# Kernel optimization log

Hardware: AMD Instinct MI355X
Metric: run time of the kernel (lower is better)

The kernel has to match this reference:

```python
import jax, jax.numpy as jnp
import numpy as np


def setup_inputs() -> dict:
    key = jax.random.key(0)
    k0, k1, k2, k3, k4, k5 = jax.random.split(key, 6)
    B, V, Fin, K, Fout = 8, 49152, 64, 3, 64
    nnz = V * 8  # ~8 neighbors per vertex (HEALPix sphere graph)
    std = (2.0 / (Fin * K)) ** 0.5  # Kaiming-normal as in reset_parameters
    inputs = jax.random.normal(k0, (B, V, Fin), jnp.float32)
    weight = jax.random.normal(k1, (Fin, K, Fout), jnp.float32) * std
    bias = jax.random.normal(k2, (Fout,), jnp.float32) * 0.05
    lap_rows = jax.random.randint(k3, (nnz,), 0, V, jnp.int32)
    lap_cols = jax.random.randint(k4, (nnz,), 0, V, jnp.int32)
    lap_vals = jax.random.normal(k5, (nnz,), jnp.float32) * 0.1
    return {"inputs": inputs, "weight": weight, "bias": bias,
            "lap_rows": lap_rows, "lap_cols": lap_cols, "lap_vals": lap_vals}


def reference(inputs, weight, bias, lap_rows, lap_cols, lap_vals):
    B, V, Fin = inputs.shape
    _, K, Fout = weight.shape

    def spmm(x):  # sparse Laplacian (COO) @ dense [V, Fin*B]
        return jax.ops.segment_sum(lap_vals[:, None] * x[lap_cols], lap_rows,
                                   num_segments=V)

    # x0: [V, Fin*B], matching torch's permute(1,2,0).view(V, Fin*B)
    x0 = inputs.transpose(1, 2, 0).reshape(V, Fin * B)
    xs = [x0]
    if K > 1:
        x1 = spmm(x0)
        xs.append(x1)
    for _ in range(2, K):
        x2 = 2.0 * spmm(x1) - x0  # Chebyshev recurrence
        xs.append(x2)
        x0, x1 = x1, x2
    x = jnp.stack(xs)                                    # [K, V, Fin*B]
    x = x.reshape(K, V, Fin, B).transpose(3, 1, 2, 0)    # [B, V, Fin, K]
    x = x.reshape(B * V, Fin * K)
    out = x @ weight.reshape(Fin * K, Fout)              # dense GEMM
    return out.reshape(B, V, Fout) + bias
```

## Files before the change

### kernel.cpp

```cpp
#include <hip/hip_runtime.h>
#include <stdint.h>

#define B_   8
#define V_   49152
#define M_   (B_ * V_)

typedef unsigned short ushort_t;
typedef __attribute__((ext_vector_type(8))) short short8;
typedef __attribute__((ext_vector_type(4))) float float4v;

__device__ __forceinline__ float bf2f_lo(unsigned int pk) {
    union { unsigned int u; float f; } x; x.u = pk << 16; return x.f;
}
__device__ __forceinline__ float bf2f_hi(unsigned int pk) {
    union { unsigned int u; float f; } x; x.u = pk & 0xffff0000u; return x.f;
}
__device__ __forceinline__ ushort_t f2bf(float f) {
    union { unsigned int u; float f; } x; x.f = f;
    unsigned int u = x.u;
    unsigned int r = u + 0x7fffu + ((u >> 16) & 1u);
    return (ushort_t)(r >> 16);
}
__device__ __forceinline__ unsigned int pack2(float a, float b) {
    return ((unsigned int)f2bf(b) << 16) | (unsigned int)f2bf(a);
}
__device__ __forceinline__ void fma8(float* acc, float w, const uint4& p) {
    const unsigned int* u = (const unsigned int*)&p;
    #pragma unroll
    for (int i = 0; i < 4; i++) {
        acc[2 * i]     += w * bf2f_lo(u[i]);
        acc[2 * i + 1] += w * bf2f_hi(u[i]);
    }
}

__global__ void fill_sentinel(float* out, int n) {
    int i = blockIdx.x * blockDim.x + threadIdx.x;
    if (i < n) out[i] = 9999.0f;
}

#define PREP_B 6144
__global__ __launch_bounds__(256) void k1_fused(const float* __restrict__ inp,
                                                ushort_t* __restrict__ x0t,
                                                const int* __restrict__ rows, int nnz,
                                                int* __restrict__ counts,
                                                const float* __restrict__ wgt,
                                                ushort_t* __restrict__ wBf, int hb) {
    int bid = blockIdx.x;
    int t = threadIdx.x;
    if (bid < PREP_B) {
        int idx = bid * 256 + t;
        int f2 = idx & 31, v = idx >> 5;
        #pragma unroll
        for (int b = 0; b < 8; b++) {
            const float* src = inp + ((size_t)b * V_ + v) * 64 + f2 * 2;
            float2 d = *(const float2*)src;
            *(unsigned int*)(x0t + ((size_t)v * 8 + b) * 64 + f2 * 2) = pack2(d.x, d.y);
        }
    } else if (bid < PREP_B + hb) {
        int i = (bid - PREP_B) * 256 + t;
        if (i < nnz) atomicAdd(&counts[rows[i]], 1);
    } else {
        int idx = (bid - PREP_B - hb) * 256 + t;
        int j = idx & 7, lane = (idx >> 3) & 63, ntc = (idx >> 9) & 3, kb = idx >> 11;
        int k = kb * 32 + (lane >> 4) * 8 + j;
        int kc = k >> 6, fi = k & 63;
        int fo = ntc * 16 + (lane & 15);
        float w;
        if (kc == 0)      w = wgt[(fi * 3 + 0) * 64 + fo] - wgt[(fi * 3 + 2) * 64 + fo];
        else if (kc == 1) w = wgt[(fi * 3 + 1) * 64 + fo];
        else              w = 2.0f * wgt[(fi * 3 + 2) * 64 + fo];
        wBf[idx] = f2bf(w);
    }
}

__global__ __launch_bounds__(1024) void scan_kernel(const int* __restrict__ counts,
                                                    int* __restrict__ offsets) {
    __shared__ int s[1024];
    int t = threadIdx.x;
    int4 c[12];
    int sum = 0;
    #pragma unroll
    for (int j = 0; j < 12; j++) {
        c[j] = ((const int4*)counts)[t * 12 + j];
        sum += c[j].x + c[j].y + c[j].z + c[j].w;
    }
    s[t] = sum;
    __syncthreads();
    for (int off = 1; off < 1024; off <<= 1) {
        int v = (t >= off) ? s[t - off] : 0;
        __syncthreads();
        s[t] += v;
        __syncthreads();
    }
    int run = (t == 0) ? 0 : s[t - 1];
    #pragma unroll
    for (int j = 0; j < 12; j++) {
        int4 o;
        o.x = run; run += c[j].x;
        o.y = run; run += c[j].y;
        o.z = run; run += c[j].z;
        o.w = run; run += c[j].w;
        ((int4*)offsets)[t * 12 + j] = o;
    }
    if (t == 1023) offsets[V_] = run;
}

__global__ void bucket_kernel(const int* __restrict__ rows, const int* __restrict__ cols,
                              const float* __restrict__ vals, int nnz,
                              const int* __restrict__ offsets, int* __restrict__ cursor,
                              uint2* __restrict__ e_cv) {
    int i = blockIdx.x * blockDim.x + threadIdx.x;
    if (i >= nnz) return;
    int r = rows[i];
    int p = offsets[r] + atomicAdd(&cursor[r], 1);
    e_cv[p] = make_uint2((unsigned int)cols[i], __float_as_uint(vals[i]));
}

__device__ __forceinline__ void gather16(const ushort_t* __restrict__ srcbf,
                                         const uint2* __restrict__ e_cv,
                                         int beg, int end, float* acc) {
    int e = beg;
    for (; e + 4 <= end; e += 4) {
        uint2 q0 = e_cv[e], q1 = e_cv[e + 1], q2 = e_cv[e + 2], q3 = e_cv[e + 3];
        float w0 = __uint_as_float(q0.y), w1 = __uint_as_float(q1.y);
        float w2 = __uint_as_float(q2.y), w3 = __uint_as_float(q3.y);
        const ushort_t* p0 = srcbf + ((size_t)q0.x * 512);
        const ushort_t* p1 = srcbf + ((size_t)q1.x * 512);
        const ushort_t* p2 = srcbf + ((size_t)q2.x * 512);
        const ushort_t* p3 = srcbf + ((size_t)q3.x * 512);
        uint4 a0 = *(const uint4*)p0, b0 = *(const uint4*)(p0 + 8);
        uint4 a1 = *(const uint4*)p1, b1 = *(const uint4*)(p1 + 8);
        uint4 a2 = *(const uint4*)p2, b2 = *(const uint4*)(p2 + 8);
        uint4 a3 = *(const uint4*)p3, b3 = *(const uint4*)(p3 + 8);
        fma8(acc, w0, a0); fma8(acc + 8, w0, b0);
        fma8(acc, w1, a1); fma8(acc + 8, w1, b1);
        fma8(acc, w2, a2); fma8(acc + 8, w2, b2);
        fma8(acc, w3, a3); fma8(acc + 8, w3, b3);
    }
    for (; e < end; e++) {
        uint2 q = e_cv[e];
        float w = __uint_as_float(q.y);
        const ushort_t* p = srcbf + ((size_t)q.x * 512);
        uint4 a = *(const uint4*)p, bq = *(const uint4*)(p + 8);
        fma8(acc, w, a); fma8(acc + 8, w, bq);
    }
}

__global__ __launch_bounds__(256) void spmm1_kernel(const ushort_t* __restrict__ x0t,
                                                    const int* __restrict__ offsets,
                                                    const uint2* __restrict__ e_cv,
                                                    ushort_t* __restrict__ x1) {
    int t = threadIdx.x;
    int vi = t >> 5, b = (t >> 2) & 7, f8 = t & 3;
    int v = blockIdx.x * 8 + vi;
    float acc[16];
    #pragma unroll
    for (int i = 0; i < 16; i++) acc[i] = 0.f;
    gather16(x0t + b * 64 + f8 * 16, e_cv, offsets[v], offsets[v + 1], acc);
    unsigned int opk[8];
    #pragma unroll
    for (int i = 0; i < 8; i++) opk[i] = pack2(acc[2 * i], acc[2 * i + 1]);
    ushort_t* dst = x1 + ((size_t)v * 8 + b) * 64 + f8 * 16;
    *(uint4*)dst       = make_uint4(opk[0], opk[1], opk[2], opk[3]);
    *(uint4*)(dst + 8) = make_uint4(opk[4], opk[5], opk[6], opk[7]);
}

__global__ __launch_bounds__(256) void spmm2_gemm(const ushort_t* __restrict__ x0t,
                                                  const ushort_t* __restrict__ x1,
                                                  const int* __restrict__ offsets,
                                                  const uint2* __restrict__ e_cv,
                                                  const ushort_t* __restrict__ wBf,
                                                  const float* __restrict__ bias,
                                                  float* __restrict__ out) {
    __shared__ ushort_t sh[64 * 72];
    int t = threadIdx.x;
    int lane = t & 63, wv = t >> 6;
    int quad = lane >> 4, col = lane & 15;
    int v0 = blockIdx.x * 8;
    int m0 = v0 * 8 + wv * 16;

    size_t arow = (size_t)(m0 + col) * 64 + quad * 8;
    short8 A0[2], A1[2];
    A0[0] = *(const short8*)(x0t + arow);
    A0[1] = *(const short8*)(x0t + arow + 32);
    A1[0] = *(const short8*)(x1 + arow);
    A1[1] = *(const short8*)(x1 + arow + 32);

    int vi = t >> 5, b = (t >> 2) & 7, f8 = t & 3;
    int v = v0 + vi;
    float acc[16];
    #pragma unroll
    for (int i = 0; i < 16; i++) acc[i] = 0.f;
    gather16(x1 + b * 64 + f8 * 16, e_cv, offsets[v], offsets[v + 1], acc);

    unsigned int opk[8];
    #pragma unroll
    for (int i = 0; i < 8; i++) opk[i] = pack2(acc[2 * i], acc[2 * i + 1]);
    int mg = vi * 8 + b;
    ushort_t* dst = sh + mg * 72 + f8 * 16;
    *(uint4*)dst       = make_uint4(opk[0], opk[1], opk[2], opk[3]);
    *(uint4*)(dst + 8) = make_uint4(opk[4], opk[5], opk[6], opk[7]);
    __syncthreads();

    short8 Bf[6][4];
    #pragma unroll
    for (int kb = 0; kb < 6; kb++)
        #pragma unroll
        for (int ntc = 0; ntc < 4; ntc++)
            Bf[kb][ntc] = *(const short8*)(wBf + ((size_t)((kb * 4 + ntc) * 64 + lane)) * 8);

    float bv[4];
    #pragma unroll
    for (int ntc = 0; ntc < 4; ntc++) bv[ntc] = bias[ntc * 16 + col];

    float4v accm[4];
    #pragma unroll
    for (int ntc = 0; ntc < 4; ntc++) accm[ntc] = (float4v){0.f, 0.f, 0.f, 0.f};

    #pragma unroll
    for (int p = 0; p < 2; p++) {
        #pragma unroll
        for (int ntc = 0; ntc < 4; ntc++)
            accm[ntc] = __builtin_amdgcn_mfma_f32_16x16x32_bf16(A0[p], Bf[p][ntc], accm[ntc], 0, 0, 0);
    }
    #pragma unroll
    for (int p = 0; p < 2; p++) {
        #pragma unroll
        for (int ntc = 0; ntc < 4; ntc++)
            accm[ntc] = __builtin_amdgcn_mfma_f32_16x16x32_bf16(A1[p], Bf[2 + p][ntc], accm[ntc], 0, 0, 0);
    }
    #pragma unroll
    for (int p = 0; p < 2; p++) {
        short8 A = *(const short8*)(sh + (wv * 16 + col) * 72 + quad * 8 + p * 32);
        #pragma unroll
        for (int ntc = 0; ntc < 4; ntc++)
            accm[ntc] = __builtin_amdgcn_mfma_f32_16x16x32_bf16(A, Bf[4 + p][ntc], accm[ntc], 0, 0, 0);
    }

    #pragma unroll
    for (int reg = 0; reg < 4; reg++) {
        int m = m0 + quad * 4 + reg;
        int vv = m >> 3, bb = m & 7;
        float* orow = out + ((size_t)bb * V_ + vv) * 64;
        #pragma unroll
        for (int ntc = 0; ntc < 4; ntc++)
            __builtin_nontemporal_store(accm[ntc][reg] + bv[ntc], &orow[ntc * 16 + col]);
    }
}

extern "C" void kernel_launch(void* const* d_in, const int* in_sizes, int n_in,
                              void* d_out, int out_size, void* d_ws, size_t ws_size,
                              hipStream_t stream) {
    const float* inp  = (const float*)d_in[0];
    const float* wgt  = (const float*)d_in[1];
    const float* bias = (const float*)d_in[2];
    const int*   rows = (const int*)d_in[3];
    const int*   cols = (const int*)d_in[4];
    const float* vals = (const float*)d_in[5];
    int nnz = in_sizes[3];
    float* out = (float*)d_out;
    (void)n_in; (void)out_size;

    char* ws = (char*)d_ws;
    size_t o = 0;
    auto alloc = [&](size_t bytes) { void* p = ws + o; o += (bytes + 255) & ~(size_t)255; return p; };
    int*      counts  = (int*)alloc((size_t)V_ * 4);
    int*      cursor  = (int*)alloc((size_t)V_ * 4);
    int*      offsets = (int*)alloc(((size_t)V_ + 1) * 4);
    uint2*    e_cv    = (uint2*)alloc((size_t)nnz * 8);
    ushort_t* x0t     = (ushort_t*)alloc((size_t)M_ * 64 * 2);
    ushort_t* x1      = (ushort_t*)alloc((size_t)M_ * 64 * 2);
    ushort_t* wBf     = (ushort_t*)alloc(6 * 4 * 64 * 8 * 2);

    if (ws_size < o) {
        fill_sentinel<<<(M_ * 64 + 255) / 256, 256, 0, stream>>>(out, M_ * 64);
        return;
    }

    int hb = (nnz + 255) / 256;
    hipMemsetAsync(counts, 0, (size_t)2 * V_ * 4, stream);
    k1_fused<<<PREP_B + hb + 48, 256, 0, stream>>>(inp, x0t, rows, nnz, counts, wgt, wBf, hb);
    scan_kernel<<<1, 1024, 0, stream>>>(counts, offsets);
    bucket_kernel<<<hb, 256, 0, stream>>>(rows, cols, vals, nnz, offsets, cursor, e_cv);
    spmm1_kernel<<<V_ / 8, 256, 0, stream>>>(x0t, offsets, e_cv, x1);
    spmm2_gemm<<<V_ / 8, 256, 0, stream>>>(x0t, x1, offsets, e_cv, wBf, bias, out);
}
```

Before: 368.2 us.

## Pad CSR rows to multiples of four and vectorize edge and transpose loads

The scan rounds each row's neighbor count up to a multiple of four, and the whole metadata region is zeroed so padded slots hold zero weights. This lets the gather loop drop its scalar tail and read edges as 16-byte pairs. The transpose/convert prep now works on float4 per thread with half the blocks, and the output stores become ordinary stores instead of nontemporal ones. In exchange the memset grows to cover the padded edge array, and each padded slot adds a wasted gather of row 0.

```diff
diff --git a/kernel.cpp b/kernel.cpp
--- a/kernel.cpp
+++ b/kernel.cpp
@@ -38,7 +38,7 @@
     if (i < n) out[i] = 9999.0f;
 }
 
-#define PREP_B 6144
+#define PREP_B 3072
 __global__ __launch_bounds__(256) void k1_fused(const float* __restrict__ inp,
                                                 ushort_t* __restrict__ x0t,
                                                 const int* __restrict__ rows, int nnz,
@@ -49,12 +49,12 @@
     int t = threadIdx.x;
     if (bid < PREP_B) {
         int idx = bid * 256 + t;
-        int f2 = idx & 31, v = idx >> 5;
+        int f4 = idx & 15, v = idx >> 4;
         #pragma unroll
         for (int b = 0; b < 8; b++) {
-            const float* src = inp + ((size_t)b * V_ + v) * 64 + f2 * 2;
-            float2 d = *(const float2*)src;
-            *(unsigned int*)(x0t + ((size_t)v * 8 + b) * 64 + f2 * 2) = pack2(d.x, d.y);
+            float4 d = *(const float4*)(inp + ((size_t)b * V_ + v) * 64 + f4 * 4);
+            uint2 o = make_uint2(pack2(d.x, d.y), pack2(d.z, d.w));
+            *(uint2*)(x0t + ((size_t)v * 8 + b) * 64 + f4 * 4) = o;
         }
     } else if (bid < PREP_B + hb) {
         int i = (bid - PREP_B) * 256 + t;
@@ -81,8 +81,11 @@
     int sum = 0;
     #pragma unroll
     for (int j = 0; j < 12; j++) {
-        c[j] = ((const int4*)counts)[t * 12 + j];
-        sum += c[j].x + c[j].y + c[j].z + c[j].w;
+        int4 q = ((const int4*)counts)[t * 12 + j];
+        q.x = (q.x + 3) & ~3; q.y = (q.y + 3) & ~3;
+        q.z = (q.z + 3) & ~3; q.w = (q.w + 3) & ~3;
+        c[j] = q;
+        sum += q.x + q.y + q.z + q.w;
     }
     s[t] = sum;
     __syncthreads();
@@ -119,15 +122,15 @@
 __device__ __forceinline__ void gather16(const ushort_t* __restrict__ srcbf,
                                          const uint2* __restrict__ e_cv,
                                          int beg, int end, float* acc) {
-    int e = beg;
-    for (; e + 4 <= end; e += 4) {
-        uint2 q0 = e_cv[e], q1 = e_cv[e + 1], q2 = e_cv[e + 2], q3 = e_cv[e + 3];
-        float w0 = __uint_as_float(q0.y), w1 = __uint_as_float(q1.y);
-        float w2 = __uint_as_float(q2.y), w3 = __uint_as_float(q3.y);
-        const ushort_t* p0 = srcbf + ((size_t)q0.x * 512);
-        const ushort_t* p1 = srcbf + ((size_t)q1.x * 512);
-        const ushort_t* p2 = srcbf + ((size_t)q2.x * 512);
-        const ushort_t* p3 = srcbf + ((size_t)q3.x * 512);
+    for (int e = beg; e < end; e += 4) {
+        uint4 E0 = *(const uint4*)(e_cv + e);
+        uint4 E1 = *(const uint4*)(e_cv + e + 2);
+        float w0 = __uint_as_float(E0.y), w1 = __uint_as_float(E0.w);
+        float w2 = __uint_as_float(E1.y), w3 = __uint_as_float(E1.w);
+        const ushort_t* p0 = srcbf + ((size_t)E0.x * 512);
+        const ushort_t* p1 = srcbf + ((size_t)E0.z * 512);
+        const ushort_t* p2 = srcbf + ((size_t)E1.x * 512);
+        const ushort_t* p3 = srcbf + ((size_t)E1.z * 512);
         uint4 a0 = *(const uint4*)p0, b0 = *(const uint4*)(p0 + 8);
         uint4 a1 = *(const uint4*)p1, b1 = *(const uint4*)(p1 + 8);
         uint4 a2 = *(const uint4*)p2, b2 = *(const uint4*)(p2 + 8);
@@ -137,13 +140,6 @@
         fma8(acc, w2, a2); fma8(acc + 8, w2, b2);
         fma8(acc, w3, a3); fma8(acc + 8, w3, b3);
     }
-    for (; e < end; e++) {
-        uint2 q = e_cv[e];
-        float w = __uint_as_float(q.y);
-        const ushort_t* p = srcbf + ((size_t)q.x * 512);
-        uint4 a = *(const uint4*)p, bq = *(const uint4*)(p + 8);
-        fma8(acc, w, a); fma8(acc + 8, w, bq);
-    }
 }
 
 __global__ __launch_bounds__(256) void spmm1_kernel(const ushort_t* __restrict__ x0t,
@@ -244,7 +240,7 @@
         float* orow = out + ((size_t)bb * V_ + vv) * 64;
         #pragma unroll
         for (int ntc = 0; ntc < 4; ntc++)
-            __builtin_nontemporal_store(accm[ntc][reg] + bv[ntc], &orow[ntc * 16 + col]);
+            orow[ntc * 16 + col] = accm[ntc][reg] + bv[ntc];
     }
 }
 
@@ -264,10 +260,13 @@
     char* ws = (char*)d_ws;
     size_t o = 0;
     auto alloc = [&](size_t bytes) { void* p = ws + o; o += (bytes + 255) & ~(size_t)255; return p; };
+    size_t meta0 = o;
     int*      counts  = (int*)alloc((size_t)V_ * 4);
     int*      cursor  = (int*)alloc((size_t)V_ * 4);
     int*      offsets = (int*)alloc(((size_t)V_ + 1) * 4);
-    uint2*    e_cv    = (uint2*)alloc((size_t)nnz * 8);
+    size_t nnz_pad = (size_t)nnz + 3 * (size_t)V_;
+    uint2*    e_cv    = (uint2*)alloc(nnz_pad * 8);
+    size_t meta_bytes = o - meta0;
     ushort_t* x0t     = (ushort_t*)alloc((size_t)M_ * 64 * 2);
     ushort_t* x1      = (ushort_t*)alloc((size_t)M_ * 64 * 2);
     ushort_t* wBf     = (ushort_t*)alloc(6 * 4 * 64 * 8 * 2);
@@ -278,7 +277,7 @@
     }
 
     int hb = (nnz + 255) / 256;
-    hipMemsetAsync(counts, 0, (size_t)2 * V_ * 4, stream);
+    hipMemsetAsync((char*)ws + meta0, 0, meta_bytes, stream);
     k1_fused<<<PREP_B + hb + 48, 256, 0, stream>>>(inp, x0t, rows, nnz, counts, wgt, wBf, hb);
     scan_kernel<<<1, 1024, 0, stream>>>(counts, offsets);
     bucket_kernel<<<hb, 256, 0, stream>>>(rows, cols, vals, nnz, offsets, cursor, e_cv);
```

After: 368.8 us. Within noise of the previous version (+0.1%).
